# Kernel optimization log

Hardware: AMD Instinct MI355X
Metric: run time of the kernel (lower is better)

The kernel has to match this reference:

```python
import jax, jax.numpy as jnp
import numpy as np

N = 50000        # nodes
E = 800000       # edges
IN_C = 128       # in_channels
HID = 256        # hidden_channels
HEADS = 4
HD = HID // HEADS
LAYERS = 4
GRAPHS = 64
OUT_C = 32
MAX_POS = 10
EPS = 1e-5


def layer_norm(x, g, b):
    mu = jnp.mean(x, axis=-1, keepdims=True)
    var = jnp.mean((x - mu) ** 2, axis=-1, keepdims=True)
    return (x - mu) / jnp.sqrt(var + EPS) * g + b


def setup_inputs() -> dict:
    key = jax.random.key(0)
    ks = jax.random.split(key, 32)
    s = 0.02
    inp = {
        "x": jax.random.normal(ks[0], (N, IN_C), dtype=jnp.float32),
        "edge_index": jax.random.randint(ks[1], (2, E), 0, N, dtype=jnp.int32),
        "pos_idx": jax.random.randint(ks[2], (N,), 0, MAX_POS, dtype=jnp.int32),
        "batch": jnp.sort(jax.random.randint(ks[3], (N,), 0, GRAPHS, dtype=jnp.int32)),
        # encoder MLP: Linear(IN->HID), ReLU, LN(HID), Linear(HID->HID); weights stored [in,out]
        "enc_w1": jax.random.normal(ks[4], (IN_C, HID)) * s,
        "enc_b1": jnp.zeros((HID,), jnp.float32),
        "enc_g": jnp.ones((HID,), jnp.float32),
        "enc_beta": jnp.zeros((HID,), jnp.float32),
        "enc_w2": jax.random.normal(ks[5], (HID, HID)) * s,
        "enc_b2": jnp.zeros((HID,), jnp.float32),
        "pos_emb": jax.random.normal(ks[6], (MAX_POS, HID)) * s,
        # stacked attention-layer params [LAYERS, ...]
        "Wq": jax.random.normal(ks[7], (LAYERS, HID, HID)) * s,
        "bq": jnp.zeros((LAYERS, HID), jnp.float32),
        "Wk": jax.random.normal(ks[8], (LAYERS, HID, HID)) * s,
        "bk": jnp.zeros((LAYERS, HID), jnp.float32),
        "Wv": jax.random.normal(ks[9], (LAYERS, HID, HID)) * s,
        "bv": jnp.zeros((LAYERS, HID), jnp.float32),
        "mlp_w1": jax.random.normal(ks[10], (LAYERS, 2 * HID, HID)) * s,
        "mlp_b1": jnp.zeros((LAYERS, HID), jnp.float32),
        "mlp_g": jnp.ones((LAYERS, HID), jnp.float32),
        "mlp_beta": jnp.zeros((LAYERS, HID), jnp.float32),
        "mlp_w2": jax.random.normal(ks[11], (LAYERS, HID, HID)) * s,
        "mlp_b2": jnp.zeros((LAYERS, HID), jnp.float32),
        # classifier
        "cls_w1": jax.random.normal(ks[12], (HID, HID)) * s,
        "cls_b1": jnp.zeros((HID,), jnp.float32),
        "cls_g": jnp.ones((HID,), jnp.float32),
        "cls_beta": jnp.zeros((HID,), jnp.float32),
        "cls_w2": jax.random.normal(ks[13], (HID, OUT_C)) * s,
        "cls_b2": jnp.zeros((OUT_C,), jnp.float32),
    }
    return inp


def reference(x, edge_index, pos_idx, batch,
              enc_w1, enc_b1, enc_g, enc_beta, enc_w2, enc_b2, pos_emb,
              Wq, bq, Wk, bk, Wv, bv,
              mlp_w1, mlp_b1, mlp_g, mlp_beta, mlp_w2, mlp_b2,
              cls_w1, cls_b1, cls_g, cls_beta, cls_w2, cls_b2):
    row, col = edge_index[0], edge_index[1]
    n = x.shape[0]
    e = row.shape[0]

    # NodeEncoder
    h = layer_norm(jax.nn.relu(x @ enc_w1 + enc_b1), enc_g, enc_beta) @ enc_w2 + enc_b2
    h = h + pos_emb[pos_idx]

    scale = jnp.asarray(HD, h.dtype) ** 0.5
    for l in range(LAYERS):
        Q = (h @ Wq[l] + bq[l]).reshape(n, HEADS, HD)
        K = (h @ Wk[l] + bk[l]).reshape(n, HEADS, HD)
        V = (h @ Wv[l] + bv[l]).reshape(n, HEADS, HD)
        # per-edge attention scores [E, HEADS]
        scores = jnp.sum(Q[row] * K[col], axis=-1) / scale
        # segment softmax over destination node `row`
        m = jax.ops.segment_max(scores, row, num_segments=n)
        ex = jnp.exp(scores - m[row])
        denom = jax.ops.segment_sum(ex, row, num_segments=n)
        w = ex / denom[row]                         # [E, HEADS]
        msg = (w[..., None] * V[col]).reshape(e, HID)
        agg = jax.ops.segment_sum(msg, row, num_segments=n)  # [N, HID]
        cat = jnp.concatenate([h, agg], axis=-1)
        z = layer_norm(jax.nn.relu(cat @ mlp_w1[l] + mlp_b1[l]), mlp_g[l], mlp_beta[l]) @ mlp_w2[l] + mlp_b2[l]
        h = z + h

    # global mean pool over graphs
    sums = jax.ops.segment_sum(h, batch, num_segments=GRAPHS)
    cnt = jax.ops.segment_sum(jnp.ones((n, 1), h.dtype), batch, num_segments=GRAPHS)
    pooled = sums / jnp.maximum(cnt, 1.0)

    out = layer_norm(jax.nn.relu(pooled @ cls_w1 + cls_b1), cls_g, cls_beta) @ cls_w2 + cls_b2
    return out
```

## Files before the change

### kernel.cpp

```cpp
#include <hip/hip_runtime.h>
#include <cstdint>

#define HID 256
#define HEADS 4
#define GRAPHS 64
#define OUTC 32
#define EPSV 1e-5f
#define PSPLIT 32

typedef __bf16 b16x8 __attribute__((ext_vector_type(8)));
typedef float  f32x4 __attribute__((ext_vector_type(4)));

__device__ __forceinline__ f32x4 mfma16(b16x8 a, b16x8 b, f32x4 c) {
    return __builtin_amdgcn_mfma_f32_16x16x32_bf16(a, b, c, 0, 0, 0);
}

__device__ __forceinline__ unsigned int pack_bf16(float a, float b) {
    unsigned short ua = __builtin_bit_cast(unsigned short, (__bf16)a);
    unsigned short ub = __builtin_bit_cast(unsigned short, (__bf16)b);
    return (unsigned int)ua | ((unsigned int)ub << 16);
}

__device__ __forceinline__ void unpack2(unsigned int u, float& lo, float& hi) {
    lo = __builtin_bit_cast(float, u << 16);
    hi = __builtin_bit_cast(float, u & 0xffff0000u);
}

__global__ __launch_bounds__(256) void wtrans_kernel(const float* __restrict__ W,
    unsigned short* __restrict__ Wt, int K, int C)
{
    __shared__ float tile[32][33];
    const float* Wm = W + (size_t)blockIdx.z * K * C;
    unsigned short* Wtm = Wt + (size_t)blockIdx.z * K * C;
    int k0 = blockIdx.x * 32, c0 = blockIdx.y * 32;
    int tx = threadIdx.x & 31, ty = threadIdx.x >> 5;
#pragma unroll
    for (int i = 0; i < 32; i += 8)
        tile[ty + i][tx] = Wm[(size_t)(k0 + ty + i) * C + c0 + tx];
    __syncthreads();
#pragma unroll
    for (int i = 0; i < 32; i += 8) {
        float v = tile[tx][ty + i];
        Wtm[(size_t)(c0 + ty + i) * K + k0 + tx] =
            __builtin_bit_cast(unsigned short, (__bf16)v);
    }
}

__global__ __launch_bounds__(256) void enc1_mfma(
    const float* __restrict__ in0, const unsigned short* __restrict__ Wt,
    const float* __restrict__ bias, const float* __restrict__ g,
    const float* __restrict__ be, unsigned short* __restrict__ outb, int n)
{
    constexpr int KTILE = 128, ROWB = 256;
    __shared__ __align__(16) char alds[64 * 256];
    __shared__ float red[4][64][2];
    int tid = threadIdx.x, lane = tid & 63, wv = tid >> 6;
    int cg = lane & 15, rg = lane >> 4;
    int base = blockIdx.x * 64;
    int cbase = wv * 64;

    f32x4 acc[4][4];
#pragma unroll
    for (int m = 0; m < 4; m++)
#pragma unroll
        for (int f = 0; f < 4; f++) acc[m][f] = (f32x4){0.f, 0.f, 0.f, 0.f};

#pragma unroll
    for (int i = 0; i < 8; i++) {
        int idx = (i * 256 + tid) * 4;
        int row = idx >> 7, k = idx & 127;
        int node = base + row;
        float4 v = {0.f, 0.f, 0.f, 0.f};
        if (node < n) v = *(const float4*)(in0 + (size_t)node * KTILE + k);
        uint2 pp; pp.x = pack_bf16(v.x, v.y); pp.y = pack_bf16(v.z, v.w);
        int off = row * ROWB + k * 2;
        off ^= (row & 7) << 4;
        *(uint2*)(alds + off) = pp;
    }
    __syncthreads();

#pragma unroll 2
    for (int k0 = 0; k0 < KTILE; k0 += 32) {
        b16x8 a[4], b[4];
#pragma unroll
        for (int m = 0; m < 4; m++) {
            int R = m * 16 + cg;
            int off = R * ROWB + (k0 + rg * 8) * 2;
            off ^= (R & 7) << 4;
            a[m] = __builtin_bit_cast(b16x8, *(const uint4*)(alds + off));
        }
#pragma unroll
        for (int f = 0; f < 4; f++) {
            const unsigned short* p = Wt + (size_t)(cbase + f * 16 + cg) * KTILE + k0 + rg * 8;
            b[f] = __builtin_bit_cast(b16x8, *(const uint4*)p);
        }
#pragma unroll
        for (int m = 0; m < 4; m++)
#pragma unroll
            for (int f = 0; f < 4; f++)
                acc[m][f] = mfma16(a[m], b[f], acc[m][f]);
    }

    float bias_v[4], g_v[4], be_v[4];
#pragma unroll
    for (int f = 0; f < 4; f++) {
        int col = cbase + f * 16 + cg;
        bias_v[f] = bias[col]; g_v[f] = g[col]; be_v[f] = be[col];
    }
#pragma unroll
    for (int m = 0; m < 4; m++)
#pragma unroll
        for (int f = 0; f < 4; f++)
#pragma unroll
            for (int r = 0; r < 4; r++)
                acc[m][f][r] = fmaxf(acc[m][f][r] + bias_v[f], 0.f);
#pragma unroll
    for (int m = 0; m < 4; m++)
#pragma unroll
        for (int r = 0; r < 4; r++) {
            float s = acc[m][0][r] + acc[m][1][r] + acc[m][2][r] + acc[m][3][r];
            float q = acc[m][0][r] * acc[m][0][r] + acc[m][1][r] * acc[m][1][r]
                    + acc[m][2][r] * acc[m][2][r] + acc[m][3][r] * acc[m][3][r];
#pragma unroll
            for (int o = 1; o < 16; o <<= 1) {
                s += __shfl_xor(s, o, 64); q += __shfl_xor(q, o, 64);
            }
            if (cg == 0) { int R = m * 16 + rg * 4 + r; red[wv][R][0] = s; red[wv][R][1] = q; }
        }
    __syncthreads();
#pragma unroll
    for (int m = 0; m < 4; m++)
#pragma unroll
        for (int r = 0; r < 4; r++) {
            int R = m * 16 + rg * 4 + r;
            float S = red[0][R][0] + red[1][R][0] + red[2][R][0] + red[3][R][0];
            float Q = red[0][R][1] + red[1][R][1] + red[2][R][1] + red[3][R][1];
            float mu = S * (1.f / HID);
            float rs = rsqrtf(Q * (1.f / HID) - mu * mu + EPSV);
            int row = base + R;
            if (row >= n) continue;
            size_t ro = (size_t)row * HID;
#pragma unroll
            for (int f = 0; f < 4; f++) {
                float v = (acc[m][f][r] - mu) * rs * g_v[f] + be_v[f];
                outb[ro + cbase + f * 16 + cg] = __builtin_bit_cast(unsigned short, (__bf16)v);
            }
        }
}

template<int KTILE, int NPASS, bool RELU_LN, bool ADD_RES, bool POS, bool OUTF, bool OUTB>
__global__ __launch_bounds__(256) void gemm_bf16(
    const unsigned short* __restrict__ in0, const unsigned short* __restrict__ in1,
    const unsigned short* __restrict__ Wt, const float* __restrict__ bias,
    const float* __restrict__ g, const float* __restrict__ be,
    const float* __restrict__ addsrc, const float* __restrict__ pos_emb,
    const int* __restrict__ pidx, float* __restrict__ outf,
    unsigned short* __restrict__ outb, int n)
{
    constexpr int KS = KTILE * NPASS;
    constexpr int ROWB = KTILE * 2;
    constexpr int UPR = KTILE / 8;
    __shared__ __align__(16) char alds[64 * KTILE * 2];
    __shared__ float red[4][64][2];

    int tid = threadIdx.x, lane = tid & 63, wv = tid >> 6;
    int cg = lane & 15, rg = lane >> 4;
    int base = blockIdx.x * 64;
    int cbase = wv * 64;

    f32x4 acc[4][4];
#pragma unroll
    for (int m = 0; m < 4; m++)
#pragma unroll
        for (int f = 0; f < 4; f++) acc[m][f] = (f32x4){0.f, 0.f, 0.f, 0.f};

    for (int pass = 0; pass < NPASS; pass++) {
        if (pass) __syncthreads();
        const unsigned short* src = pass ? in1 : in0;
        constexpr int ITERS = (64 * UPR) / 256;
#pragma unroll
        for (int i = 0; i < ITERS; i++) {
            int idx = i * 256 + tid;
            int row = idx / UPR, u = idx % UPR;
            int node = base + row;
            uint4 v = {0u, 0u, 0u, 0u};
            if (node < n) v = *(const uint4*)(src + (size_t)node * KTILE + u * 8);
            int off = row * ROWB + u * 16;
            off ^= (row & 7) << 4;
            *(uint4*)(alds + off) = v;
        }
        __syncthreads();

        const unsigned short* Wp = Wt + pass * KTILE;
#pragma unroll 2
        for (int k0 = 0; k0 < KTILE; k0 += 32) {
            b16x8 a[4], b[4];
#pragma unroll
            for (int m = 0; m < 4; m++) {
                int R = m * 16 + cg;
                int off = R * ROWB + (k0 + rg * 8) * 2;
                off ^= (R & 7) << 4;
                a[m] = __builtin_bit_cast(b16x8, *(const uint4*)(alds + off));
            }
#pragma unroll
            for (int f = 0; f < 4; f++) {
                const unsigned short* p = Wp + (size_t)(cbase + f * 16 + cg) * KS + k0 + rg * 8;
                b[f] = __builtin_bit_cast(b16x8, *(const uint4*)p);
            }
#pragma unroll
            for (int m = 0; m < 4; m++)
#pragma unroll
                for (int f = 0; f < 4; f++)
                    acc[m][f] = mfma16(a[m], b[f], acc[m][f]);
        }
    }

    float bias_v[4], g_v[4], be_v[4];
#pragma unroll
    for (int f = 0; f < 4; f++) {
        int col = cbase + f * 16 + cg;
        bias_v[f] = bias[col];
        if (RELU_LN) { g_v[f] = g[col]; be_v[f] = be[col]; }
    }
#pragma unroll
    for (int m = 0; m < 4; m++)
#pragma unroll
        for (int f = 0; f < 4; f++)
#pragma unroll
            for (int r = 0; r < 4; r++) acc[m][f][r] += bias_v[f];

    if (RELU_LN) {
#pragma unroll
        for (int m = 0; m < 4; m++)
#pragma unroll
            for (int f = 0; f < 4; f++)
#pragma unroll
                for (int r = 0; r < 4; r++) acc[m][f][r] = fmaxf(acc[m][f][r], 0.f);
#pragma unroll
        for (int m = 0; m < 4; m++)
#pragma unroll
            for (int r = 0; r < 4; r++) {
                float s = acc[m][0][r] + acc[m][1][r] + acc[m][2][r] + acc[m][3][r];
                float q = acc[m][0][r] * acc[m][0][r] + acc[m][1][r] * acc[m][1][r]
                        + acc[m][2][r] * acc[m][2][r] + acc[m][3][r] * acc[m][3][r];
#pragma unroll
                for (int o = 1; o < 16; o <<= 1) {
                    s += __shfl_xor(s, o, 64); q += __shfl_xor(q, o, 64);
                }
                if (cg == 0) { int R = m * 16 + rg * 4 + r; red[wv][R][0] = s; red[wv][R][1] = q; }
            }
        __syncthreads();
#pragma unroll
        for (int m = 0; m < 4; m++)
#pragma unroll
            for (int r = 0; r < 4; r++) {
                int R = m * 16 + rg * 4 + r;
                float S = red[0][R][0] + red[1][R][0] + red[2][R][0] + red[3][R][0];
                float Q = red[0][R][1] + red[1][R][1] + red[2][R][1] + red[3][R][1];
                float mu = S * (1.f / HID);
                float rs = rsqrtf(Q * (1.f / HID) - mu * mu + EPSV);
#pragma unroll
                for (int f = 0; f < 4; f++)
                    acc[m][f][r] = (acc[m][f][r] - mu) * rs * g_v[f] + be_v[f];
            }
    }

#pragma unroll
    for (int m = 0; m < 4; m++)
#pragma unroll
        for (int r = 0; r < 4; r++) {
            int row = base + m * 16 + rg * 4 + r;
            if (row >= n) continue;
            size_t ro = (size_t)row * HID;
            int pid = 0;
            if (POS) pid = pidx[row];
#pragma unroll
            for (int f = 0; f < 4; f++) {
                int col = cbase + f * 16 + cg;
                float v = acc[m][f][r];
                if (ADD_RES) v += addsrc[ro + col];
                if (POS)     v += pos_emb[(size_t)pid * HID + col];
                if (OUTF)    outf[ro + col] = v;
                if (OUTB)    outb[ro + col] = __builtin_bit_cast(unsigned short, (__bf16)v);
            }
        }
}

__global__ __launch_bounds__(256) void qkv_mfma_kernel(
    const unsigned short* __restrict__ hsrc,
    const unsigned short* __restrict__ Wtq, const unsigned short* __restrict__ Wtk,
    const unsigned short* __restrict__ Wtv,
    const float* __restrict__ bq, const float* __restrict__ bk, const float* __restrict__ bv,
    unsigned short* __restrict__ Qo, unsigned short* __restrict__ Ko,
    unsigned short* __restrict__ Vo, int n)
{
    constexpr int ROWB = 512;
    __shared__ __align__(16) char alds[64 * 512];
    int tid = threadIdx.x, lane = tid & 63, wv = tid >> 6;
    int cg = lane & 15, rg = lane >> 4;
    int base = blockIdx.x * 64;
    int cbase = wv * 64;

#pragma unroll
    for (int i = 0; i < 8; i++) {
        int idx = i * 256 + tid;
        int row = idx >> 5, u = idx & 31;
        int node = base + row;
        uint4 v = {0u, 0u, 0u, 0u};
        if (node < n) v = *(const uint4*)(hsrc + (size_t)node * HID + u * 8);
        int off = row * ROWB + u * 16;
        off ^= (row & 7) << 4;
        *(uint4*)(alds + off) = v;
    }
    __syncthreads();

    for (int mat = 0; mat < 3; mat++) {
        const unsigned short* Wp = (mat == 0) ? Wtq : (mat == 1) ? Wtk : Wtv;
        const float* bp = (mat == 0) ? bq : (mat == 1) ? bk : bv;
        unsigned short* op = (mat == 0) ? Qo : (mat == 1) ? Ko : Vo;

        f32x4 acc[4][4];
#pragma unroll
        for (int m = 0; m < 4; m++)
#pragma unroll
            for (int f = 0; f < 4; f++) acc[m][f] = (f32x4){0.f, 0.f, 0.f, 0.f};

#pragma unroll 2
        for (int k0 = 0; k0 < 256; k0 += 32) {
            b16x8 a[4], b[4];
#pragma unroll
            for (int m = 0; m < 4; m++) {
                int R = m * 16 + cg;
                int off = R * ROWB + (k0 + rg * 8) * 2;
                off ^= (R & 7) << 4;
                a[m] = __builtin_bit_cast(b16x8, *(const uint4*)(alds + off));
            }
#pragma unroll
            for (int f = 0; f < 4; f++) {
                const unsigned short* p = Wp + (size_t)(cbase + f * 16 + cg) * 256 + k0 + rg * 8;
                b[f] = __builtin_bit_cast(b16x8, *(const uint4*)p);
            }
#pragma unroll
            for (int m = 0; m < 4; m++)
#pragma unroll
                for (int f = 0; f < 4; f++)
                    acc[m][f] = mfma16(a[m], b[f], acc[m][f]);
        }

        float bias_v[4];
#pragma unroll
        for (int f = 0; f < 4; f++) bias_v[f] = bp[cbase + f * 16 + cg];
#pragma unroll
        for (int m = 0; m < 4; m++)
#pragma unroll
            for (int r = 0; r < 4; r++) {
                int row = base + m * 16 + rg * 4 + r;
                if (row >= n) continue;
                size_t ro = (size_t)row * HID;
#pragma unroll
                for (int f = 0; f < 4; f++) {
                    float v = acc[m][f][r] + bias_v[f];
                    op[ro + cbase + f * 16 + cg] = __builtin_bit_cast(unsigned short, (__bf16)v);
                }
            }
    }
}

__global__ void count_kernel(const int* __restrict__ row, int* __restrict__ counts, int e)
{
    int i = blockIdx.x * blockDim.x + threadIdx.x;
    if (i < e) atomicAdd(&counts[row[i]], 1);
}

__global__ __launch_bounds__(256) void scan1_kernel(const int* __restrict__ counts,
    int* __restrict__ offs, int* __restrict__ bsum, int n)
{
    __shared__ int wsumS[4];
    int tid = threadIdx.x, b = blockIdx.x;
    int i = b * 256 + tid;
    int v = (i < n) ? counts[i] : 0;
    int lane = tid & 63, wv = tid >> 6;
    int s = v;
#pragma unroll
    for (int o = 1; o < 64; o <<= 1) { int t = __shfl_up(s, o, 64); if (lane >= o) s += t; }
    if (lane == 63) wsumS[wv] = s;
    __syncthreads();
    int add = 0;
    for (int j = 0; j < wv; j++) add += wsumS[j];
    s += add;
    if (i < n) offs[i + 1] = s;
    if (tid == 255) bsum[b] = s;
}

__global__ __launch_bounds__(256) void scan2_kernel(int* __restrict__ bsum, int nb)
{
    __shared__ int wsumS[4];
    int tid = threadIdx.x;
    int v = (tid < nb) ? bsum[tid] : 0;
    int lane = tid & 63, wv = tid >> 6;
    int s = v;
#pragma unroll
    for (int o = 1; o < 64; o <<= 1) { int t = __shfl_up(s, o, 64); if (lane >= o) s += t; }
    if (lane == 63) wsumS[wv] = s;
    __syncthreads();
    int add = 0;
    for (int j = 0; j < wv; j++) add += wsumS[j];
    s += add;
    if (tid < nb) bsum[tid] = s;
}

__global__ __launch_bounds__(256) void scan3_kernel(int* __restrict__ offs,
    const int* __restrict__ bsum, int n)
{
    int tid = threadIdx.x, b = blockIdx.x;
    int i = b * 256 + tid;
    if (i == 0) offs[0] = 0;
    if (i < n && b > 0) offs[i + 1] += bsum[b - 1];
}

__global__ void scatter_kernel(const int* __restrict__ row, const int* __restrict__ col,
    const int* __restrict__ offs, int* __restrict__ cur, int* __restrict__ ccol, int e)
{
    int i = blockIdx.x * blockDim.x + threadIdx.x;
    if (i >= e) return;
    int r = row[i];
    int pos = atomicAdd(&cur[r], 1);
    ccol[offs[r] + pos] = col[i];
}

__global__ __launch_bounds__(256) void attn_bf16_kernel(
    const unsigned short* __restrict__ Qm, const unsigned short* __restrict__ Km,
    const unsigned short* __restrict__ Vm,
    const int* __restrict__ offs, const int* __restrict__ ccol,
    unsigned short* __restrict__ agg, int n)
{
    __shared__ float accT[8][HID];
    __shared__ float wredM[8][HEADS];
    __shared__ float wredD[8][HEADS];
    int node = blockIdx.x;
    int tid = threadIdx.x, lane = tid & 63, wv = tid >> 6;
    int hw = (wv << 1) | (lane >> 5);
    int l32 = lane & 31;
    int grp = l32 >> 3;
    int start = offs[node], fin = offs[node + 1];
    if (fin == start) {
        agg[(size_t)node * HID + tid] = 0;
        return;
    }

    uint4 qr = *(const uint4*)(Qm + (size_t)node * HID + l32 * 8);
    float qf[8];
    unpack2(qr.x, qf[0], qf[1]);
    unpack2(qr.y, qf[2], qf[3]);
    unpack2(qr.z, qf[4], qf[5]);
    unpack2(qr.w, qf[6], qf[7]);

    float m = -3.0e38f, d = 0.f;
    float acc[8];
#pragma unroll
    for (int j = 0; j < 8; j++) acc[j] = 0.f;

    for (int i = start + hw; i < fin; i += 8) {
        int c = ccol[i];
        uint4 kr = *(const uint4*)(Km + (size_t)c * HID + l32 * 8);
        float k0, k1, k2, k3, k4, k5, k6, k7;
        unpack2(kr.x, k0, k1); unpack2(kr.y, k2, k3);
        unpack2(kr.z, k4, k5); unpack2(kr.w, k6, k7);
        float p = qf[0] * k0 + qf[1] * k1 + qf[2] * k2 + qf[3] * k3
                + qf[4] * k4 + qf[5] * k5 + qf[6] * k6 + qf[7] * k7;
        p += __shfl_xor(p, 1, 64);
        p += __shfl_xor(p, 2, 64);
        p += __shfl_xor(p, 4, 64);
        float s = p * 0.125f;
        float mn = fmaxf(m, s);
        float sc = __expf(m - mn);
        float w = __expf(s - mn);
        d = d * sc + w;
        uint4 vr = *(const uint4*)(Vm + (size_t)c * HID + l32 * 8);
        float v0, v1, v2, v3, v4, v5, v6, v7;
        unpack2(vr.x, v0, v1); unpack2(vr.y, v2, v3);
        unpack2(vr.z, v4, v5); unpack2(vr.w, v6, v7);
        acc[0] = acc[0] * sc + w * v0;  acc[1] = acc[1] * sc + w * v1;
        acc[2] = acc[2] * sc + w * v2;  acc[3] = acc[3] * sc + w * v3;
        acc[4] = acc[4] * sc + w * v4;  acc[5] = acc[5] * sc + w * v5;
        acc[6] = acc[6] * sc + w * v6;  acc[7] = acc[7] * sc + w * v7;
        m = mn;
    }
    if ((l32 & 7) == 0) { wredM[hw][grp] = m; wredD[hw][grp] = d; }
    __syncthreads();
    float M = wredM[0][grp];
#pragma unroll
    for (int j = 1; j < 8; j++) M = fmaxf(M, wredM[j][grp]);
    float fac = __expf(m - M);
    float4 a0 = {acc[0] * fac, acc[1] * fac, acc[2] * fac, acc[3] * fac};
    float4 a1 = {acc[4] * fac, acc[5] * fac, acc[6] * fac, acc[7] * fac};
    *(float4*)&accT[hw][l32 * 8]     = a0;
    *(float4*)&accT[hw][l32 * 8 + 4] = a1;
    __syncthreads();
    int hh = tid >> 6;
    float M2 = wredM[0][hh];
#pragma unroll
    for (int j = 1; j < 8; j++) M2 = fmaxf(M2, wredM[j][hh]);
    float D = 0.f;
#pragma unroll
    for (int j = 0; j < 8; j++) D += wredD[j][hh] * __expf(wredM[j][hh] - M2);
    float r = 0.f;
#pragma unroll
    for (int j = 0; j < 8; j++) r += accT[j][tid];
    agg[(size_t)node * HID + tid] = __builtin_bit_cast(unsigned short, (__bf16)(r / D));
}

__global__ void bounds_kernel(const int* __restrict__ batch, int* __restrict__ gb, int n)
{
    int g = threadIdx.x;
    if (g > GRAPHS) return;
    int lo = 0, hi = n;
    while (lo < hi) { int mid = (lo + hi) >> 1; if (batch[mid] < g) lo = mid + 1; else hi = mid; }
    gb[g] = lo;
}

__global__ __launch_bounds__(256) void pool_partial_kernel(const float* __restrict__ h,
    const int* __restrict__ gb, float* __restrict__ partial)
{
    int s = blockIdx.x, g = blockIdx.y, tid = threadIdx.x;
    int lo = gb[g], hi = gb[g + 1];
    float sum = 0.f;
    for (int i = lo + s; i < hi; i += PSPLIT) sum += h[(size_t)i * HID + tid];
    partial[((size_t)g * PSPLIT + s) * HID + tid] = sum;
}

__global__ __launch_bounds__(256) void pool_reduce_kernel(const float* __restrict__ partial,
    const int* __restrict__ gb, float* __restrict__ pooled)
{
    int g = blockIdx.x, tid = threadIdx.x;
    float sum = 0.f;
#pragma unroll
    for (int s = 0; s < PSPLIT; s++) sum += partial[((size_t)g * PSPLIT + s) * HID + tid];
    int cnt = gb[g + 1] - gb[g];
    pooled[g * HID + tid] = sum / fmaxf((float)cnt, 1.f);
}

__global__ __launch_bounds__(256) void cls_kernel(const float* __restrict__ pooled,
    const float* __restrict__ W1, const float* __restrict__ b1,
    const float* __restrict__ g, const float* __restrict__ be,
    const float* __restrict__ W2, const float* __restrict__ b2,
    float* __restrict__ out)
{
    __shared__ float pin[HID];
    __shared__ float hbuf[HID];
    __shared__ float red2[4][2];
    int tid = threadIdx.x, gi = blockIdx.x;
    int lane = tid & 63, wv = tid >> 6;
    pin[tid] = pooled[gi * HID + tid];
    __syncthreads();
    float acc = 0.f;
    for (int k = 0; k < HID; k++) acc += pin[k] * W1[k * HID + tid];
    acc = fmaxf(acc + b1[tid], 0.f);
    float s = acc, q = acc * acc;
#pragma unroll
    for (int o = 1; o < 64; o <<= 1) { s += __shfl_xor(s, o, 64); q += __shfl_xor(q, o, 64); }
    if (lane == 0) { red2[wv][0] = s; red2[wv][1] = q; }
    __syncthreads();
    float S = red2[0][0] + red2[1][0] + red2[2][0] + red2[3][0];
    float Q = red2[0][1] + red2[1][1] + red2[2][1] + red2[3][1];
    float mu = S * (1.f / HID);
    float rs = rsqrtf(Q * (1.f / HID) - mu * mu + EPSV);
    hbuf[tid] = (acc - mu) * rs * g[tid] + be[tid];
    __syncthreads();
    if (tid < OUTC) {
        float o = 0.f;
        for (int k = 0; k < HID; k++) o += hbuf[k] * W2[k * OUTC + tid];
        out[gi * OUTC + tid] = o + b2[tid];
    }
}

extern "C" void kernel_launch(void* const* d_in, const int* in_sizes, int n_in,
                              void* d_out, int out_size, void* d_ws, size_t ws_size,
                              hipStream_t stream)
{
    const float* x        = (const float*)d_in[0];
    const int*   ei       = (const int*)d_in[1];
    const int*   pidx     = (const int*)d_in[2];
    const int*   batch    = (const int*)d_in[3];
    const float* enc_w1   = (const float*)d_in[4];
    const float* enc_b1   = (const float*)d_in[5];
    const float* enc_g    = (const float*)d_in[6];
    const float* enc_beta = (const float*)d_in[7];
    const float* enc_w2   = (const float*)d_in[8];
    const float* enc_b2   = (const float*)d_in[9];
    const float* pos_emb  = (const float*)d_in[10];
    const float* Wq       = (const float*)d_in[11];
    const float* bq       = (const float*)d_in[12];
    const float* Wk       = (const float*)d_in[13];
    const float* bk       = (const float*)d_in[14];
    const float* Wv       = (const float*)d_in[15];
    const float* bv       = (const float*)d_in[16];
    const float* mlp_w1   = (const float*)d_in[17];
    const float* mlp_b1   = (const float*)d_in[18];
    const float* mlp_g    = (const float*)d_in[19];
    const float* mlp_beta = (const float*)d_in[20];
    const float* mlp_w2   = (const float*)d_in[21];
    const float* mlp_b2   = (const float*)d_in[22];
    const float* cls_w1   = (const float*)d_in[23];
    const float* cls_b1   = (const float*)d_in[24];
    const float* cls_g    = (const float*)d_in[25];
    const float* cls_beta = (const float*)d_in[26];
    const float* cls_w2   = (const float*)d_in[27];
    const float* cls_b2   = (const float*)d_in[28];

    int n = in_sizes[2];
    int e = in_sizes[1] / 2;
    const int* row = ei;
    const int* col = ei + e;

    char* p = (char*)d_ws;
    auto alloc = [&](size_t bytes) -> void* {
        void* r = (void*)p;
        p += (bytes + 255) & ~(size_t)255;
        return r;
    };
    size_t NH = (size_t)n * HID;
    float* h             = (float*)alloc(NH * 4);
    unsigned short* h16  = (unsigned short*)alloc(NH * 2);
    unsigned short* a16  = (unsigned short*)alloc(NH * 2);
    unsigned short* m16  = (unsigned short*)alloc(NH * 2);
    unsigned short* Qb   = (unsigned short*)alloc(NH * 2);
    unsigned short* Kb   = (unsigned short*)alloc(NH * 2);
    unsigned short* Vb   = (unsigned short*)alloc(NH * 2);
    float* partial = (float*)alloc((size_t)GRAPHS * PSPLIT * HID * 4);
    float* pooled  = (float*)alloc((size_t)GRAPHS * HID * 4);
    int* counts = (int*)alloc((size_t)n * 4);
    int* offs   = (int*)alloc((size_t)(n + 1) * 4);
    int* cur    = (int*)alloc((size_t)n * 4);
    int* ccol   = (int*)alloc((size_t)e * 4);
    int* bsum   = (int*)alloc(1024);
    int* gb     = (int*)alloc((GRAPHS + 1) * 4);
    unsigned short* wt_e1 = (unsigned short*)alloc((size_t)128 * 256 * 2);
    unsigned short* wt_e2 = (unsigned short*)alloc((size_t)256 * 256 * 2);
    unsigned short* wt_q  = (unsigned short*)alloc((size_t)4 * 256 * 256 * 2);
    unsigned short* wt_k  = (unsigned short*)alloc((size_t)4 * 256 * 256 * 2);
    unsigned short* wt_v  = (unsigned short*)alloc((size_t)4 * 256 * 256 * 2);
    unsigned short* wt_m1 = (unsigned short*)alloc((size_t)4 * 512 * 256 * 2);
    unsigned short* wt_m2 = (unsigned short*)alloc((size_t)4 * 256 * 256 * 2);

    int gblocks = (n + 63) / 64;
    int nb = (n + 255) / 256;

    wtrans_kernel<<<dim3(4, 8, 1),  256, 0, stream>>>(enc_w1, wt_e1, 128, 256);
    wtrans_kernel<<<dim3(8, 8, 1),  256, 0, stream>>>(enc_w2, wt_e2, 256, 256);
    wtrans_kernel<<<dim3(8, 8, 4),  256, 0, stream>>>(Wq,     wt_q,  256, 256);
    wtrans_kernel<<<dim3(8, 8, 4),  256, 0, stream>>>(Wk,     wt_k,  256, 256);
    wtrans_kernel<<<dim3(8, 8, 4),  256, 0, stream>>>(Wv,     wt_v,  256, 256);
    wtrans_kernel<<<dim3(16, 8, 4), 256, 0, stream>>>(mlp_w1, wt_m1, 512, 256);
    wtrans_kernel<<<dim3(8, 8, 4),  256, 0, stream>>>(mlp_w2, wt_m2, 256, 256);

    hipMemsetAsync(counts, 0, (size_t)n * 4, stream);
    hipMemsetAsync(cur, 0, (size_t)n * 4, stream);
    count_kernel<<<(e + 255) / 256, 256, 0, stream>>>(row, counts, e);
    scan1_kernel<<<nb, 256, 0, stream>>>(counts, offs, bsum, n);
    scan2_kernel<<<1, 256, 0, stream>>>(bsum, nb);
    scan3_kernel<<<nb, 256, 0, stream>>>(offs, bsum, n);
    scatter_kernel<<<(e + 255) / 256, 256, 0, stream>>>(row, col, offs, cur, ccol, e);
    bounds_kernel<<<1, 128, 0, stream>>>(batch, gb, n);

    enc1_mfma<<<gblocks, 256, 0, stream>>>(x, wt_e1, enc_b1, enc_g, enc_beta, m16, n);
    gemm_bf16<256, 1, false, false, true, true, true><<<gblocks, 256, 0, stream>>>(
        m16, nullptr, wt_e2, enc_b2, nullptr, nullptr, nullptr, pos_emb, pidx, h, h16, n);

    for (int l = 0; l < 4; l++) {
        size_t wo = (size_t)l * 256 * 256;
        size_t bo = (size_t)l * HID;
        qkv_mfma_kernel<<<gblocks, 256, 0, stream>>>(
            h16, wt_q + wo, wt_k + wo, wt_v + wo, bq + bo, bk + bo, bv + bo,
            Qb, Kb, Vb, n);
        attn_bf16_kernel<<<n, 256, 0, stream>>>(Qb, Kb, Vb, offs, ccol, a16, n);
        gemm_bf16<256, 2, true, false, false, false, true><<<gblocks, 256, 0, stream>>>(
            h16, a16, wt_m1 + (size_t)l * 512 * 256, mlp_b1 + bo,
            mlp_g + bo, mlp_beta + bo, nullptr, nullptr, nullptr, nullptr, m16, n);
        gemm_bf16<256, 1, false, true, false, true, true><<<gblocks, 256, 0, stream>>>(
            m16, nullptr, wt_m2 + wo, mlp_b2 + bo, nullptr, nullptr, h, nullptr, nullptr,
            h, h16, n);
    }

    pool_partial_kernel<<<dim3(PSPLIT, GRAPHS), 256, 0, stream>>>(h, gb, partial);
    pool_reduce_kernel<<<GRAPHS, 256, 0, stream>>>(partial, gb, pooled);
    cls_kernel<<<GRAPHS, 256, 0, stream>>>(pooled, cls_w1, cls_b1, cls_g, cls_beta,
                                           cls_w2, cls_b2, (float*)d_out);
}
```

Baseline: 1.419 ms.

## Map one half-wave per destination node in edge attention kernel

Rewrites the attention aggregation so that each 32-lane half-wave handles a whole destination node serially over its edges, with 8 nodes per block. Previously each block handled one node with its 8 half-waves splitting the edges. That required shared-memory online-softmax merging across half-waves and two block barriers. Removing the cross-wave reduction and syncs cuts per-node overhead and block count; K and V loads are also issued together. The tradeoff is less parallelism for high-degree nodes and load imbalance within a block.

```diff
diff --git a/kernel.cpp b/kernel.cpp
--- a/kernel.cpp
+++ b/kernel.cpp
@@ -428,27 +428,26 @@
     ccol[offs[r] + pos] = col[i];
 }
 
-__global__ __launch_bounds__(256) void attn_bf16_kernel(
+__global__ __launch_bounds__(256) void attn_hw_kernel(
     const unsigned short* __restrict__ Qm, const unsigned short* __restrict__ Km,
     const unsigned short* __restrict__ Vm,
     const int* __restrict__ offs, const int* __restrict__ ccol,
     unsigned short* __restrict__ agg, int n)
 {
-    __shared__ float accT[8][HID];
-    __shared__ float wredM[8][HEADS];
-    __shared__ float wredD[8][HEADS];
-    int node = blockIdx.x;
-    int tid = threadIdx.x, lane = tid & 63, wv = tid >> 6;
-    int hw = (wv << 1) | (lane >> 5);
-    int l32 = lane & 31;
-    int grp = l32 >> 3;
+    int tid = threadIdx.x;
+    int hw = tid >> 5;
+    int l32 = tid & 31;
+    int node = blockIdx.x * 8 + hw;
+    if (node >= n) return;
     int start = offs[node], fin = offs[node + 1];
-    if (fin == start) {
-        agg[(size_t)node * HID + tid] = 0;
+    size_t rowoff = (size_t)node * HID + l32 * 8;
+    if (start == fin) {
+        uint4 z = {0u, 0u, 0u, 0u};
+        *(uint4*)(agg + rowoff) = z;
         return;
     }
 
-    uint4 qr = *(const uint4*)(Qm + (size_t)node * HID + l32 * 8);
+    uint4 qr = *(const uint4*)(Qm + rowoff);
     float qf[8];
     unpack2(qr.x, qf[0], qf[1]);
     unpack2(qr.y, qf[2], qf[3]);
@@ -460,9 +459,12 @@
 #pragma unroll
     for (int j = 0; j < 8; j++) acc[j] = 0.f;
 
-    for (int i = start + hw; i < fin; i += 8) {
+    for (int i = start; i < fin; i++) {
         int c = ccol[i];
-        uint4 kr = *(const uint4*)(Km + (size_t)c * HID + l32 * 8);
+        const unsigned short* kp = Km + (size_t)c * HID + l32 * 8;
+        const unsigned short* vp = Vm + (size_t)c * HID + l32 * 8;
+        uint4 kr = *(const uint4*)kp;
+        uint4 vr = *(const uint4*)vp;
         float k0, k1, k2, k3, k4, k5, k6, k7;
         unpack2(kr.x, k0, k1); unpack2(kr.y, k2, k3);
         unpack2(kr.z, k4, k5); unpack2(kr.w, k6, k7);
@@ -476,7 +478,6 @@
         float sc = __expf(m - mn);
         float w = __expf(s - mn);
         d = d * sc + w;
-        uint4 vr = *(const uint4*)(Vm + (size_t)c * HID + l32 * 8);
         float v0, v1, v2, v3, v4, v5, v6, v7;
         unpack2(vr.x, v0, v1); unpack2(vr.y, v2, v3);
         unpack2(vr.z, v4, v5); unpack2(vr.w, v6, v7);
@@ -486,28 +487,14 @@
         acc[6] = acc[6] * sc + w * v6;  acc[7] = acc[7] * sc + w * v7;
         m = mn;
     }
-    if ((l32 & 7) == 0) { wredM[hw][grp] = m; wredD[hw][grp] = d; }
-    __syncthreads();
-    float M = wredM[0][grp];
-#pragma unroll
-    for (int j = 1; j < 8; j++) M = fmaxf(M, wredM[j][grp]);
-    float fac = __expf(m - M);
-    float4 a0 = {acc[0] * fac, acc[1] * fac, acc[2] * fac, acc[3] * fac};
-    float4 a1 = {acc[4] * fac, acc[5] * fac, acc[6] * fac, acc[7] * fac};
-    *(float4*)&accT[hw][l32 * 8]     = a0;
-    *(float4*)&accT[hw][l32 * 8 + 4] = a1;
-    __syncthreads();
-    int hh = tid >> 6;
-    float M2 = wredM[0][hh];
-#pragma unroll
-    for (int j = 1; j < 8; j++) M2 = fmaxf(M2, wredM[j][hh]);
-    float D = 0.f;
-#pragma unroll
-    for (int j = 0; j < 8; j++) D += wredD[j][hh] * __expf(wredM[j][hh] - M2);
-    float r = 0.f;
-#pragma unroll
-    for (int j = 0; j < 8; j++) r += accT[j][tid];
-    agg[(size_t)node * HID + tid] = __builtin_bit_cast(unsigned short, (__bf16)(r / D));
+
+    float inv = 1.f / d;
+    uint4 out;
+    out.x = pack_bf16(acc[0] * inv, acc[1] * inv);
+    out.y = pack_bf16(acc[2] * inv, acc[3] * inv);
+    out.z = pack_bf16(acc[4] * inv, acc[5] * inv);
+    out.w = pack_bf16(acc[6] * inv, acc[7] * inv);
+    *(uint4*)(agg + rowoff) = out;
 }
 
 __global__ void bounds_kernel(const int* __restrict__ batch, int* __restrict__ gb, int n)
@@ -667,13 +654,14 @@
     gemm_bf16<256, 1, false, false, true, true, true><<<gblocks, 256, 0, stream>>>(
         m16, nullptr, wt_e2, enc_b2, nullptr, nullptr, nullptr, pos_emb, pidx, h, h16, n);
 
+    int ablocks = (n + 7) / 8;
     for (int l = 0; l < 4; l++) {
         size_t wo = (size_t)l * 256 * 256;
         size_t bo = (size_t)l * HID;
         qkv_mfma_kernel<<<gblocks, 256, 0, stream>>>(
             h16, wt_q + wo, wt_k + wo, wt_v + wo, bq + bo, bk + bo, bv + bo,
             Qb, Kb, Vb, n);
-        attn_bf16_kernel<<<n, 256, 0, stream>>>(Qb, Kb, Vb, offs, ccol, a16, n);
+        attn_hw_kernel<<<ablocks, 256, 0, stream>>>(Qb, Kb, Vb, offs, ccol, a16, n);
         gemm_bf16<256, 2, true, false, false, false, true><<<gblocks, 256, 0, stream>>>(
             h16, a16, wt_m1 + (size_t)l * 512 * 256, mlp_b1 + bo,
             mlp_g + bo, mlp_beta + bo, nullptr, nullptr, nullptr, nullptr, m16, n);
```

Result: no change. 1.431 ms (+0.8%).
